# Kernel tuning notes

Measured on AMD Instinct MI355X. Metric: run time of the kernel, lower is better.

The kernel has to match this reference:

```python
import jax, jax.numpy as jnp
import numpy as np

# PGA G(3,0,1) blade basis, standard ordering
BLADES = [(), (0,), (1,), (2,), (3,), (0,1), (0,2), (0,3), (1,2), (1,3), (2,3),
          (0,1,2), (0,1,3), (0,2,3), (1,2,3), (0,1,2,3)]
IDX = {b: i for i, b in enumerate(BLADES)}
METRIC = (0, 1, 1, 1)  # e0^2 = 0, e1^2 = e2^2 = e3^2 = 1


def _mul(a, b, wedge=False):
    """Product of basis blades; returns (sign, blade) with sign 0 if vanishing."""
    s = list(a) + list(b)
    sign = 1
    changed = True
    while changed:  # bubble sort, counting swaps
        changed = False
        for i in range(len(s) - 1):
            if s[i] > s[i + 1]:
                s[i], s[i + 1] = s[i + 1], s[i]
                sign = -sign
                changed = True
    out, i = [], 0
    while i < len(s):
        if i + 1 < len(s) and s[i] == s[i + 1]:
            if wedge:
                return 0, None
            sign *= METRIC[s[i]]
            i += 2
        else:
            out.append(s[i]); i += 1
    if sign == 0:
        return 0, None
    return sign, tuple(out)


def _build_cayley(wedge):
    C = np.zeros((16, 16, 16), np.float32)
    for i, a in enumerate(BLADES):
        for j, b in enumerate(BLADES):
            s, r = _mul(a, b, wedge=wedge)
            if s:
                C[i, j, IDX[r]] = s
    return C


def _build_dual():
    """dual(x) = D @ x with a ^ dual(a) = e0123."""
    D = np.zeros((16, 16), np.float32)
    full = (0, 1, 2, 3)
    for i, a in enumerate(BLADES):
        comp = tuple(x for x in full if x not in a)
        s, r = _mul(a, comp, wedge=True)
        assert r == full
        D[IDX[comp], i] = s
    return D


def _build_basis():
    """9 equivariant linear basis maps: 5 grade projections + 4 e0-multiplications."""
    maps = []
    for g in range(5):
        M = np.zeros((16, 16), np.float32)
        for i, b in enumerate(BLADES):
            if len(b) == g:
                M[i, i] = 1.0
        maps.append(M)
    for g in range(4):
        M = np.zeros((16, 16), np.float32)
        for i, b in enumerate(BLADES):
            if len(b) == g and 0 not in b:
                s, r = _mul((0,), b)
                M[IDX[r], i] = s
        maps.append(M)
    return np.stack(maps)  # [9, 16, 16]


_GP = jnp.asarray(_build_cayley(False))
_WEDGE = jnp.asarray(_build_cayley(True))
_DUAL_NP = _build_dual()
_DUAL = jnp.asarray(_DUAL_NP)
_UNDUAL = jnp.asarray(np.linalg.inv(_DUAL_NP).astype(np.float32))
_BASIS = jnp.asarray(_build_basis())


def equi_linear(x, w):
    # x: [B, P, in, 16], w: [out, in, 9] -> [B, P, out, 16]
    wk = jnp.einsum('oib,bkl->oikl', w, _BASIS)
    return jnp.einsum('oikl,BPil->BPok', wk, x)


def geometric_product(x, y):
    return jnp.einsum('ijk,BPci,BPcj->BPck', _GP, x, y)


def equi_join(x, y, ref):
    dx = jnp.einsum('kl,BPcl->BPck', _DUAL, x)
    dy = jnp.einsum('kl,BPcl->BPck', _DUAL, y)
    w = jnp.einsum('ijk,BPci,BPcj->BPck', _WEDGE, dx, dy)
    j = jnp.einsum('kl,BPcl->BPck', _UNDUAL, w)
    return j * ref[..., 15:16]  # scale by reference pseudoscalar (equivariance fix)


def setup_inputs() -> dict:
    key = jax.random.key(0)
    k1, k2, k3, k4 = jax.random.split(key, 4)
    B, P, C_hidden, C_inter = 64, 1024, 48, 48
    hidden = jax.random.normal(k1, (B, P, C_hidden, 16), dtype=jnp.float32)
    ref = jax.random.normal(k2, (B, 1, 1, 16), dtype=jnp.float32)
    scale_b = 1.0 / np.sqrt(C_hidden * 9)
    scale_n = 1.0 / np.sqrt(C_inter * 9)
    w_bili = jax.random.normal(k3, (2 * C_inter, C_hidden, 9), dtype=jnp.float32) * scale_b
    w_next = jax.random.normal(k4, (C_hidden, C_inter, 9), dtype=jnp.float32) * scale_n
    return {"hidden": hidden, "ref": ref, "w_bili": w_bili, "w_next": w_next}


def reference(hidden, ref, w_bili, w_next):
    h = equi_linear(hidden, w_bili)              # [B, P, 96, 16]
    lg, rg, lj, rj = jnp.split(h, 4, axis=-2)    # each [B, P, 24, 16]
    gp = geometric_product(lg, rg)
    jn = equi_join(lj, rj, ref)
    out = jnp.concatenate([gp, jn], axis=-2)     # [B, P, 48, 16]
    return equi_linear(out, w_next)
```

## Files before the change

### kernel.cpp

```cpp
#include <hip/hip_runtime.h>


typedef unsigned short ushort_t;
typedef unsigned int uint_t;

constexpr unsigned char BB[16] = {
  0x0, 0x1, 0x2, 0x4, 0x8,
  0x3, 0x5, 0x9, 0x6, 0xA, 0xC,
  0x7, 0xB, 0xD, 0xE,
  0xF
};
constexpr int popc4(unsigned x){ return (x&1)+((x>>1)&1)+((x>>2)&1)+((x>>3)&1); }
constexpr int idx_of(unsigned bits){
  int r = 0;
  for (int i = 0; i < 16; ++i) if (BB[i] == bits) r = i;
  return r;
}
constexpr int reorder_sign(unsigned a, unsigned b){
  int sw = 0;
  for (int g = 0; g < 4; ++g) if (b & (1u<<g)) sw += popc4(a >> (g+1));
  return (sw & 1) ? -1 : 1;
}
struct Tab { signed char s[16][16]; signed char k[16][16]; };
constexpr Tab make_gp(){
  Tab t{};
  for (int i = 0; i < 16; ++i)
    for (int j = 0; j < 16; ++j){
      unsigned a = BB[i], b = BB[j];
      if ((a & b) & 1u) { t.s[i][j] = 0; t.k[i][j] = 0; }
      else { t.s[i][j] = (signed char)reorder_sign(a,b);
             t.k[i][j] = (signed char)idx_of(a ^ b); }
    }
  return t;
}
constexpr int d_idx(int i){ return idx_of(0xFu ^ BB[i]); }
constexpr int d_sgn(int i){ return reorder_sign(BB[i], 0xFu ^ BB[i]); }
constexpr Tab make_join(){
  Tab t{};
  for (int a = 0; a < 16; ++a)
    for (int b = 0; b < 16; ++b){
      int da = d_idx(a), db = d_idx(b);
      if (BB[da] & BB[db]) { t.s[a][b] = 0; t.k[a][b] = 0; }
      else {
        int ws = reorder_sign(BB[da], BB[db]);
        int m  = idx_of(BB[da] ^ BB[db]);
        int l  = idx_of(0xFu ^ BB[m]);
        t.s[a][b] = (signed char)(d_sgn(a) * d_sgn(b) * ws * d_sgn(l));
        t.k[a][b] = (signed char)l;
      }
    }
  return t;
}
constexpr Tab GPT = make_gp();
constexpr Tab JNT = make_join();

struct ITab { int v[16]; };
constexpr ITab make_grade(){ ITab t{}; for (int i=0;i<16;++i) t.v[i]=popc4(BB[i]); return t; }
constexpr ITab make_partner(){ ITab t{}; for (int i=0;i<16;++i) t.v[i]=idx_of(BB[i] & ~1u); return t; }
constexpr ITab GRD = make_grade();
constexpr ITab PRT = make_partner();
constexpr int KPERM[16] = {0,2,3,4,8,9,10,14,  1,5,6,7,11,12,13,15};

#define NPTS   65536
#define CIN    48
#define CH     96
#define COUT   48
#define PTS    16
#define XROWF  772
#define GSTR   272
#define BUF_F  13056
#define HROW   1540
#define OROWF  772

__global__ void prep_weights(const float* __restrict__ wb,
                             const float* __restrict__ wn,
                             float* __restrict__ W1, float* __restrict__ W2){
  int i = blockIdx.x * 256 + threadIdx.x;
  if (i < 9*CH*CIN){
    int b = i / (CH*CIN); int r = i % (CH*CIN); int o = r / CIN; int c = r % CIN;
    W1[i] = wb[(o*CIN + c)*9 + b];
  }
  if (i < 9*COUT*CIN){
    int b = i / (COUT*CIN); int r = i % (COUT*CIN); int o = r / CIN; int c = r % CIN;
    W2[i] = wn[(o*CIN + c)*9 + b];
  }
}

__global__ __launch_bounds__(256, 1)
void fused_bilinear(const float* __restrict__ x,
                    const float* __restrict__ refp,
                    const float* __restrict__ W1,
                    const float* __restrict__ W2,
                    float* __restrict__ out){
  __shared__ float buf[BUF_F];
  __shared__ float hs[PTS * HROW];

  const int t  = threadIdx.x;
  const long p0 = (long)blockIdx.x * PTS;

  for (int c = t; c < PTS * 192; c += 256){
    int p = c / 192, r = c % 192;
    float4 v = ((const float4*)(x + (p0 + p) * 768))[r];
    ((float4*)(buf + p * XROWF))[r] = v;
  }
  __syncthreads();

  {
    const int p = t & 15, slot = t >> 4;
    const int k  = KPERM[slot];
    const int b0 = GRD.v[k];
    const int kp = PRT.v[k];
    const bool has_e0 = (BB[k] & 1u) != 0;
    const float* w0 = W1 + b0 * (CH*CIN);
    const float* w1 = W1 + (4 + b0) * (CH*CIN);

    float xr[CIN];
    #pragma unroll
    for (int i = 0; i < CIN; ++i) xr[i] = buf[p*XROWF + i*16 + k];

    if (!has_e0){
      #pragma unroll 2
      for (int o = 0; o < CH; ++o){
        const float* wr = w0 + o * CIN;
        float a0=0.f,a1=0.f,a2=0.f,a3=0.f;
        #pragma unroll
        for (int i = 0; i < CIN; i += 4){
          a0 += wr[i]*xr[i];     a1 += wr[i+1]*xr[i+1];
          a2 += wr[i+2]*xr[i+2]; a3 += wr[i+3]*xr[i+3];
        }
        hs[p*HROW + o*16 + k] = (a0+a1)+(a2+a3);
      }
    } else {
      float xr2[CIN];
      #pragma unroll
      for (int i = 0; i < CIN; ++i) xr2[i] = buf[p*XROWF + i*16 + kp];
      #pragma unroll 2
      for (int o = 0; o < CH; ++o){
        const float* wr  = w0 + o * CIN;
        const float* wr2 = w1 + o * CIN;
        float a0=0.f,a1=0.f,a2=0.f,a3=0.f;
        #pragma unroll
        for (int i = 0; i < CIN; i += 4){
          a0 += wr[i]*xr[i];       a1 += wr[i+1]*xr[i+1];
          a2 += wr[i+2]*xr[i+2];   a3 += wr[i+3]*xr[i+3];
          a0 += wr2[i]*xr2[i];     a1 += wr2[i+1]*xr2[i+1];
          a2 += wr2[i+2]*xr2[i+2]; a3 += wr2[i+3]*xr2[i+3];
        }
        hs[p*HROW + o*16 + k] = (a0+a1)+(a2+a3);
      }
    }
  }
  __syncthreads();

  for (int tau = t; tau < 768; tau += 256){
    const int p = tau & 15, u = tau >> 4;
    if (u < 24){
      float lg[16], rg[16], oo[16];
      #pragma unroll
      for (int k = 0; k < 16; ++k){
        lg[k] = hs[p*HROW + u*16 + k];
        rg[k] = hs[p*HROW + (24+u)*16 + k];
        oo[k] = 0.f;
      }
      #pragma unroll
      for (int i = 0; i < 16; ++i)
        #pragma unroll
        for (int j = 0; j < 16; ++j){
          const int s = GPT.s[i][j];
          if (s > 0)      oo[GPT.k[i][j]] += lg[i]*rg[j];
          else if (s < 0) oo[GPT.k[i][j]] -= lg[i]*rg[j];
        }
      #pragma unroll
      for (int k = 0; k < 16; ++k) buf[u*GSTR + p*17 + k] = oo[k];
    } else {
      const int c = u - 24;
      float lj[16], rj[16], oo[16];
      #pragma unroll
      for (int k = 0; k < 16; ++k){
        lj[k] = hs[p*HROW + (48+c)*16 + k];
        rj[k] = hs[p*HROW + (72+c)*16 + k];
        oo[k] = 0.f;
      }
      #pragma unroll
      for (int i = 0; i < 16; ++i)
        #pragma unroll
        for (int j = 0; j < 16; ++j){
          const int s = JNT.s[i][j];
          if (s > 0)      oo[JNT.k[i][j]] += lj[i]*rj[j];
          else if (s < 0) oo[JNT.k[i][j]] -= lj[i]*rj[j];
        }
      const float rps = refp[(int)((p0 + p) >> 10) * 16 + 15];
      #pragma unroll
      for (int k = 0; k < 16; ++k) buf[u*GSTR + p*17 + k] = oo[k]*rps;
    }
  }
  __syncthreads();

  float* outS = hs;
  {
    const int p = t & 15, slot = t >> 4;
    const int k  = KPERM[slot];
    const int b0 = GRD.v[k];
    const int kp = PRT.v[k];
    const bool has_e0 = (BB[k] & 1u) != 0;
    const float* w0 = W2 + b0 * (COUT*CIN);
    const float* w1 = W2 + (4 + b0) * (COUT*CIN);

    float gr[CIN];
    #pragma unroll
    for (int c = 0; c < CIN; ++c) gr[c] = buf[c*GSTR + p*17 + k];

    if (!has_e0){
      #pragma unroll 2
      for (int o = 0; o < COUT; ++o){
        const float* wr = w0 + o * CIN;
        float a0=0.f,a1=0.f,a2=0.f,a3=0.f;
        #pragma unroll
        for (int c = 0; c < CIN; c += 4){
          a0 += wr[c]*gr[c];     a1 += wr[c+1]*gr[c+1];
          a2 += wr[c+2]*gr[c+2]; a3 += wr[c+3]*gr[c+3];
        }
        outS[p*OROWF + o*16 + k] = (a0+a1)+(a2+a3);
      }
    } else {
      float gr2[CIN];
      #pragma unroll
      for (int c = 0; c < CIN; ++c) gr2[c] = buf[c*GSTR + p*17 + kp];
      #pragma unroll 2
      for (int o = 0; o < COUT; ++o){
        const float* wr  = w0 + o * CIN;
        const float* wr2 = w1 + o * CIN;
        float a0=0.f,a1=0.f,a2=0.f,a3=0.f;
        #pragma unroll
        for (int c = 0; c < CIN; c += 4){
          a0 += wr[c]*gr[c];       a1 += wr[c+1]*gr[c+1];
          a2 += wr[c+2]*gr[c+2];   a3 += wr[c+3]*gr[c+3];
          a0 += wr2[c]*gr2[c];     a1 += wr2[c+1]*gr2[c+1];
          a2 += wr2[c+2]*gr2[c+2]; a3 += wr2[c+3]*gr2[c+3];
        }
        outS[p*OROWF + o*16 + k] = (a0+a1)+(a2+a3);
      }
    }
  }
  __syncthreads();

  for (int c = t; c < PTS * 192; c += 256){
    int p = c / 192, r = c % 192;
    float4 v = ((const float4*)(outS + p * OROWF))[r];
    ((float4*)(out + (p0 + p) * 768))[r] = v;
  }
}

extern "C" void kernel_launch(void* const* d_in, const int* in_sizes, int n_in,
                              void* d_out, int out_size, void* d_ws, size_t ws_size,
                              hipStream_t stream){
  (void)in_sizes; (void)n_in; (void)out_size; (void)ws_size;
  const float* hidden = (const float*)d_in[0];
  const float* refp   = (const float*)d_in[1];
  const float* wbili  = (const float*)d_in[2];
  const float* wnext  = (const float*)d_in[3];
  float* outp = (float*)d_out;

  float* W1 = (float*)d_ws;
  float* W2 = W1 + 9*CH*CIN;

  prep_weights<<<162, 256, 0, stream>>>(wbili, wnext, W1, W2);
  fused_bilinear<<<NPTS/PTS, 256, 0, stream>>>(hidden, refp, W1, W2, outp);
}
```

Measured before the change: 2.039 ms.

## Fuse bilinear linear map into product stage, per-channel threads, smaller tiles

Work is restructured so each thread owns one (point, channel) pair and computes its left and right hidden multivectors in registers, then applies the geometric product or join directly. This removes the large shared-memory hidden buffer and one barrier stage. Weights are re-laid out per output channel for float4 loads, the tile shrinks to 8 points, and launch bounds now allow 3 blocks per CU. In exchange, weight traffic per point rises and the smaller tile gives less reuse of each weight load, while register pressure is high.

```diff
diff --git a/kernel.cpp b/kernel.cpp
--- a/kernel.cpp
+++ b/kernel.cpp
@@ -1,8 +1,5 @@
 #include <hip/hip_runtime.h>
 
-
-typedef unsigned short ushort_t;
-typedef unsigned int uint_t;
 
 constexpr unsigned char BB[16] = {
   0x0, 0x1, 0x2, 0x4, 0x8,
@@ -57,197 +54,179 @@
 struct ITab { int v[16]; };
 constexpr ITab make_grade(){ ITab t{}; for (int i=0;i<16;++i) t.v[i]=popc4(BB[i]); return t; }
 constexpr ITab make_partner(){ ITab t{}; for (int i=0;i<16;++i) t.v[i]=idx_of(BB[i] & ~1u); return t; }
+constexpr ITab make_e0(){ ITab t{}; for (int i=0;i<16;++i) t.v[i]=(BB[i]&1u); return t; }
 constexpr ITab GRD = make_grade();
 constexpr ITab PRT = make_partner();
-constexpr int KPERM[16] = {0,2,3,4,8,9,10,14,  1,5,6,7,11,12,13,15};
+constexpr ITab E0T = make_e0();
 
 #define NPTS   65536
 #define CIN    48
 #define CH     96
 #define COUT   48
-#define PTS    16
+#define PTS    8
 #define XROWF  772
-#define GSTR   272
-#define BUF_F  13056
-#define HROW   1540
-#define OROWF  772
+#define WSTR   432
+
+__device__ __forceinline__ float f4c(const float4& v, int c){
+  return c==0 ? v.x : (c==1 ? v.y : (c==2 ? v.z : v.w));
+}
 
 __global__ void prep_weights(const float* __restrict__ wb,
                              const float* __restrict__ wn,
                              float* __restrict__ W1, float* __restrict__ W2){
   int i = blockIdx.x * 256 + threadIdx.x;
   if (i < 9*CH*CIN){
-    int b = i / (CH*CIN); int r = i % (CH*CIN); int o = r / CIN; int c = r % CIN;
+    int o = i / WSTR; int r = i % WSTR; int b = r / CIN; int c = r % CIN;
     W1[i] = wb[(o*CIN + c)*9 + b];
   }
   if (i < 9*COUT*CIN){
-    int b = i / (COUT*CIN); int r = i % (COUT*CIN); int o = r / CIN; int c = r % CIN;
+    int o = i / WSTR; int r = i % WSTR; int b = r / CIN; int c = r % CIN;
     W2[i] = wn[(o*CIN + c)*9 + b];
   }
 }
 
-__global__ __launch_bounds__(256, 1)
+__global__ __launch_bounds__(256, 3)
 void fused_bilinear(const float* __restrict__ x,
                     const float* __restrict__ refp,
                     const float* __restrict__ W1,
                     const float* __restrict__ W2,
                     float* __restrict__ out){
-  __shared__ float buf[BUF_F];
-  __shared__ float hs[PTS * HROW];
+  __shared__ float xs[PTS * XROWF];
+  __shared__ float gs[PTS * XROWF];
 
   const int t  = threadIdx.x;
   const long p0 = (long)blockIdx.x * PTS;
 
   for (int c = t; c < PTS * 192; c += 256){
     int p = c / 192, r = c % 192;
-    float4 v = ((const float4*)(x + (p0 + p) * 768))[r];
-    ((float4*)(buf + p * XROWF))[r] = v;
+    ((float4*)(xs + p * XROWF))[r] = ((const float4*)(x + (p0 + p) * 768))[r];
   }
   __syncthreads();
 
-  {
-    const int p = t & 15, slot = t >> 4;
-    const int k  = KPERM[slot];
-    const int b0 = GRD.v[k];
-    const int kp = PRT.v[k];
-    const bool has_e0 = (BB[k] & 1u) != 0;
-    const float* w0 = W1 + b0 * (CH*CIN);
-    const float* w1 = W1 + (4 + b0) * (CH*CIN);
-
-    float xr[CIN];
+  for (int tau = t; tau < PTS * 48; tau += 256){
+    const int p = tau & (PTS - 1);
+    const int c = tau >> 3;
+    const int cl = (c < 24) ? c        : (24 + c);
+    const int cr = (c < 24) ? (24 + c) : (48 + c);
+    const float* __restrict__ Wl = W1 + cl * WSTR;
+    const float* __restrict__ Wr = W1 + cr * WSTR;
+
+    float hl[16], hr[16];
     #pragma unroll
-    for (int i = 0; i < CIN; ++i) xr[i] = buf[p*XROWF + i*16 + k];
-
-    if (!has_e0){
-      #pragma unroll 2
-      for (int o = 0; o < CH; ++o){
-        const float* wr = w0 + o * CIN;
-        float a0=0.f,a1=0.f,a2=0.f,a3=0.f;
-        #pragma unroll
-        for (int i = 0; i < CIN; i += 4){
-          a0 += wr[i]*xr[i];     a1 += wr[i+1]*xr[i+1];
-          a2 += wr[i+2]*xr[i+2]; a3 += wr[i+3]*xr[i+3];
-        }
-        hs[p*HROW + o*16 + k] = (a0+a1)+(a2+a3);
-      }
-    } else {
-      float xr2[CIN];
-      #pragma unroll
-      for (int i = 0; i < CIN; ++i) xr2[i] = buf[p*XROWF + i*16 + kp];
-      #pragma unroll 2
-      for (int o = 0; o < CH; ++o){
-        const float* wr  = w0 + o * CIN;
-        const float* wr2 = w1 + o * CIN;
-        float a0=0.f,a1=0.f,a2=0.f,a3=0.f;
-        #pragma unroll
-        for (int i = 0; i < CIN; i += 4){
-          a0 += wr[i]*xr[i];       a1 += wr[i+1]*xr[i+1];
-          a2 += wr[i+2]*xr[i+2];   a3 += wr[i+3]*xr[i+3];
-          a0 += wr2[i]*xr2[i];     a1 += wr2[i+1]*xr2[i+1];
-          a2 += wr2[i+2]*xr2[i+2]; a3 += wr2[i+3]*xr2[i+3];
-        }
-        hs[p*HROW + o*16 + k] = (a0+a1)+(a2+a3);
-      }
-    }
-  }
-  __syncthreads();
-
-  for (int tau = t; tau < 768; tau += 256){
-    const int p = tau & 15, u = tau >> 4;
-    if (u < 24){
-      float lg[16], rg[16], oo[16];
-      #pragma unroll
-      for (int k = 0; k < 16; ++k){
-        lg[k] = hs[p*HROW + u*16 + k];
-        rg[k] = hs[p*HROW + (24+u)*16 + k];
-        oo[k] = 0.f;
-      }
+    for (int k = 0; k < 16; ++k){ hl[k] = 0.f; hr[k] = 0.f; }
+
+    #pragma unroll 1
+    for (int i0 = 0; i0 < CIN; i0 += 4){
+      float4 wl[9], wr[9];
+      #pragma unroll
+      for (int b = 0; b < 9; ++b){
+        wl[b] = *(const float4*)(Wl + b*CIN + i0);
+        wr[b] = *(const float4*)(Wr + b*CIN + i0);
+      }
+      #pragma unroll
+      for (int di = 0; di < 4; ++di){
+        const float* xi = xs + p * XROWF + (i0 + di) * 16;
+        const float4 x0 = *(const float4*)(xi);
+        const float4 x1 = *(const float4*)(xi + 4);
+        const float4 x2 = *(const float4*)(xi + 8);
+        const float4 x3 = *(const float4*)(xi + 12);
+        const float xv[16] = {x0.x,x0.y,x0.z,x0.w, x1.x,x1.y,x1.z,x1.w,
+                              x2.x,x2.y,x2.z,x2.w, x3.x,x3.y,x3.z,x3.w};
+        #pragma unroll
+        for (int k = 0; k < 16; ++k){
+          const float xk = xv[k];
+          hl[k] += f4c(wl[GRD.v[k]], di) * xk;
+          hr[k] += f4c(wr[GRD.v[k]], di) * xk;
+        }
+        #pragma unroll
+        for (int k = 0; k < 16; ++k){
+          if (E0T.v[k]){
+            const float xp = xv[PRT.v[k]];
+            hl[k] += f4c(wl[4 + GRD.v[k]], di) * xp;
+            hr[k] += f4c(wr[4 + GRD.v[k]], di) * xp;
+          }
+        }
+      }
+    }
+
+    float oo[16];
+    #pragma unroll
+    for (int k = 0; k < 16; ++k) oo[k] = 0.f;
+    if (c < 24){
       #pragma unroll
       for (int i = 0; i < 16; ++i)
         #pragma unroll
         for (int j = 0; j < 16; ++j){
           const int s = GPT.s[i][j];
-          if (s > 0)      oo[GPT.k[i][j]] += lg[i]*rg[j];
-          else if (s < 0) oo[GPT.k[i][j]] -= lg[i]*rg[j];
-        }
-      #pragma unroll
-      for (int k = 0; k < 16; ++k) buf[u*GSTR + p*17 + k] = oo[k];
+          if (s > 0)      oo[GPT.k[i][j]] += hl[i]*hr[j];
+          else if (s < 0) oo[GPT.k[i][j]] -= hl[i]*hr[j];
+        }
     } else {
-      const int c = u - 24;
-      float lj[16], rj[16], oo[16];
-      #pragma unroll
-      for (int k = 0; k < 16; ++k){
-        lj[k] = hs[p*HROW + (48+c)*16 + k];
-        rj[k] = hs[p*HROW + (72+c)*16 + k];
-        oo[k] = 0.f;
-      }
       #pragma unroll
       for (int i = 0; i < 16; ++i)
         #pragma unroll
         for (int j = 0; j < 16; ++j){
           const int s = JNT.s[i][j];
-          if (s > 0)      oo[JNT.k[i][j]] += lj[i]*rj[j];
-          else if (s < 0) oo[JNT.k[i][j]] -= lj[i]*rj[j];
+          if (s > 0)      oo[JNT.k[i][j]] += hl[i]*hr[j];
+          else if (s < 0) oo[JNT.k[i][j]] -= hl[i]*hr[j];
         }
       const float rps = refp[(int)((p0 + p) >> 10) * 16 + 15];
       #pragma unroll
-      for (int k = 0; k < 16; ++k) buf[u*GSTR + p*17 + k] = oo[k]*rps;
-    }
+      for (int k = 0; k < 16; ++k) oo[k] *= rps;
+    }
+    float* gp_ = gs + p * XROWF + c * 16;
+    *(float4*)(gp_ + 0)  = make_float4(oo[0], oo[1], oo[2], oo[3]);
+    *(float4*)(gp_ + 4)  = make_float4(oo[4], oo[5], oo[6], oo[7]);
+    *(float4*)(gp_ + 8)  = make_float4(oo[8], oo[9], oo[10],oo[11]);
+    *(float4*)(gp_ + 12) = make_float4(oo[12],oo[13],oo[14],oo[15]);
   }
   __syncthreads();
 
-  float* outS = hs;
-  {
-    const int p = t & 15, slot = t >> 4;
-    const int k  = KPERM[slot];
-    const int b0 = GRD.v[k];
-    const int kp = PRT.v[k];
-    const bool has_e0 = (BB[k] & 1u) != 0;
-    const float* w0 = W2 + b0 * (COUT*CIN);
-    const float* w1 = W2 + (4 + b0) * (COUT*CIN);
-
-    float gr[CIN];
+  float* outS = xs;
+  for (int tau = t; tau < PTS * 48; tau += 256){
+    const int p = tau & (PTS - 1);
+    const int o = tau >> 3;
+    const float* __restrict__ Wo = W2 + o * WSTR;
+
+    float acc[16];
     #pragma unroll
-    for (int c = 0; c < CIN; ++c) gr[c] = buf[c*GSTR + p*17 + k];
-
-    if (!has_e0){
-      #pragma unroll 2
-      for (int o = 0; o < COUT; ++o){
-        const float* wr = w0 + o * CIN;
-        float a0=0.f,a1=0.f,a2=0.f,a3=0.f;
-        #pragma unroll
-        for (int c = 0; c < CIN; c += 4){
-          a0 += wr[c]*gr[c];     a1 += wr[c+1]*gr[c+1];
-          a2 += wr[c+2]*gr[c+2]; a3 += wr[c+3]*gr[c+3];
-        }
-        outS[p*OROWF + o*16 + k] = (a0+a1)+(a2+a3);
-      }
-    } else {
-      float gr2[CIN];
-      #pragma unroll
-      for (int c = 0; c < CIN; ++c) gr2[c] = buf[c*GSTR + p*17 + kp];
-      #pragma unroll 2
-      for (int o = 0; o < COUT; ++o){
-        const float* wr  = w0 + o * CIN;
-        const float* wr2 = w1 + o * CIN;
-        float a0=0.f,a1=0.f,a2=0.f,a3=0.f;
-        #pragma unroll
-        for (int c = 0; c < CIN; c += 4){
-          a0 += wr[c]*gr[c];       a1 += wr[c+1]*gr[c+1];
-          a2 += wr[c+2]*gr[c+2];   a3 += wr[c+3]*gr[c+3];
-          a0 += wr2[c]*gr2[c];     a1 += wr2[c+1]*gr2[c+1];
-          a2 += wr2[c+2]*gr2[c+2]; a3 += wr2[c+3]*gr2[c+3];
-        }
-        outS[p*OROWF + o*16 + k] = (a0+a1)+(a2+a3);
-      }
-    }
+    for (int k = 0; k < 16; ++k) acc[k] = 0.f;
+
+    #pragma unroll 1
+    for (int c0 = 0; c0 < CIN; c0 += 4){
+      float4 w[9];
+      #pragma unroll
+      for (int b = 0; b < 9; ++b) w[b] = *(const float4*)(Wo + b*CIN + c0);
+      #pragma unroll
+      for (int dc = 0; dc < 4; ++dc){
+        const float* gi = gs + p * XROWF + (c0 + dc) * 16;
+        const float4 g0 = *(const float4*)(gi);
+        const float4 g1 = *(const float4*)(gi + 4);
+        const float4 g2 = *(const float4*)(gi + 8);
+        const float4 g3 = *(const float4*)(gi + 12);
+        const float gv[16] = {g0.x,g0.y,g0.z,g0.w, g1.x,g1.y,g1.z,g1.w,
+                              g2.x,g2.y,g2.z,g2.w, g3.x,g3.y,g3.z,g3.w};
+        #pragma unroll
+        for (int k = 0; k < 16; ++k)
+          acc[k] += f4c(w[GRD.v[k]], dc) * gv[k];
+        #pragma unroll
+        for (int k = 0; k < 16; ++k){
+          if (E0T.v[k])
+            acc[k] += f4c(w[4 + GRD.v[k]], dc) * gv[PRT.v[k]];
+        }
+      }
+    }
+    float* op_ = outS + p * XROWF + o * 16;
+    *(float4*)(op_ + 0)  = make_float4(acc[0], acc[1], acc[2], acc[3]);
+    *(float4*)(op_ + 4)  = make_float4(acc[4], acc[5], acc[6], acc[7]);
+    *(float4*)(op_ + 8)  = make_float4(acc[8], acc[9], acc[10],acc[11]);
+    *(float4*)(op_ + 12) = make_float4(acc[12],acc[13],acc[14],acc[15]);
   }
   __syncthreads();
 
   for (int c = t; c < PTS * 192; c += 256){
     int p = c / 192, r = c % 192;
-    float4 v = ((const float4*)(outS + p * OROWF))[r];
-    ((float4*)(out + (p0 + p) * 768))[r] = v;
+    ((float4*)(out + (p0 + p) * 768))[r] = ((const float4*)(outS + p * XROWF))[r];
   }
 }
 
```

Measured after the change: 2.152 ms. 5.5% more time.
